# Kernel optimization log

Measured on AMD Instinct MI355X. Metric: run time of the kernel, lower is better.

The kernel has to match this reference:

```python
import jax, jax.numpy as jnp
import numpy as np

B, L, C, K, NLEV, VOCAB, OUT = 32, 1024, 512, 2, 4, 128, 11


def setup_inputs() -> dict:
    key = jax.random.key(0)
    ks = jax.random.split(key, 8)
    x = jax.random.randint(ks[0], (B, L), 0, VOCAB, dtype=jnp.int32)
    mask = jax.random.randint(ks[1], (B, L), 0, 2).astype(jnp.bool_)
    emb = jax.random.uniform(ks[2], (VOCAB, C), minval=-0.5, maxval=0.5, dtype=jnp.float32)
    w1 = jax.random.normal(ks[3], (NLEV, C, C, K), dtype=jnp.float32) * 0.02
    b1 = jnp.zeros((NLEV, C), dtype=jnp.float32)
    w2 = jax.random.normal(ks[4], (NLEV, C, C, K), dtype=jnp.float32) * 0.02
    b2 = jnp.zeros((NLEV, C), dtype=jnp.float32)
    dec_w = jax.random.uniform(ks[5], (OUT, C), minval=-0.5, maxval=0.5, dtype=jnp.float32)
    dec_b = jnp.zeros((OUT,), dtype=jnp.float32)
    return dict(x=x, mask=mask, emb=emb, w1=w1, b1=b1, w2=w2, b2=b2, dec_w=dec_w, dec_b=dec_b)


def _causal_conv(h, w, b, dilation):
    # h: [B, C, L], w: [Cout, Cin, K]; left-pad (K-1)*d == conv+chomp in TCN
    pad = (w.shape[-1] - 1) * dilation
    out = jax.lax.conv_general_dilated(
        h, w, window_strides=(1,), padding=[(pad, 0)],
        rhs_dilation=(dilation,), dimension_numbers=("NCH", "OIH", "NCH"))
    return out + b[None, :, None]


def reference(x, mask, emb, w1, b1, w2, b2, dec_w, dec_b):
    h = emb[x].transpose(0, 2, 1)  # [B, C, L]
    for i in range(NLEV):  # fixed small number of TCN levels
        d = 2 ** i
        res = h
        h = jax.nn.relu(_causal_conv(h, w1[i], b1[i], d))
        h = jax.nn.relu(_causal_conv(h, w2[i], b2[i], d))
        h = jax.nn.relu(h + res)  # residual (in==out channels -> identity shortcut)
    y = jnp.einsum("bcl,oc->blo", h, dec_w) + dec_b  # [B, L, OUT]
    # mask-gather: original keeps only mask-true positions; zero others (jit-safe)
    return y * mask[..., None].astype(y.dtype)
```

## Files before the change

kernel.cpp:

```cpp
#include <hip/hip_runtime.h>
#include <stdint.h>

#define BB 32
#define LL 1024
#define CC 512
#define NN (BB * LL)
#define NLEVS 4
#define OUTD 11
#define LPAD 8
#define LROWS (LL + LPAD)

typedef __attribute__((ext_vector_type(8))) short bf16x8;
typedef __attribute__((ext_vector_type(4))) float f32x4;

static __device__ __forceinline__ unsigned short f2bf(float f) {
    union { float f; uint32_t u; } v; v.f = f;
    uint32_t u = v.u;
    uint32_t r = (u + 0x7fffu + ((u >> 16) & 1u)) >> 16;
    return (unsigned short)r;
}
static __device__ __forceinline__ float bf2f(unsigned short h) {
    union { uint32_t u; float f; } v; v.u = ((uint32_t)h) << 16;
    return v.f;
}

static __device__ __forceinline__ void llds16(const unsigned short* g, unsigned short* l) {
    __builtin_amdgcn_global_load_lds(
        (const __attribute__((address_space(1))) unsigned int*)g,
        (__attribute__((address_space(3))) unsigned int*)l, 16, 0, 0);
}

__global__ __launch_bounds__(256) void prep_kernel(
    const int* __restrict__ x, const float* __restrict__ emb,
    const float* __restrict__ w1, const float* __restrict__ w2,
    const float* __restrict__ dw,
    unsigned short* __restrict__ Hb0, unsigned short* __restrict__ Hb1,
    unsigned short* __restrict__ WpT, unsigned short* __restrict__ dwp)
{
    int b = blockIdx.x;
    if (b < 16384) {
        int e = b * 256 + threadIdx.x;
        int cv = e >> 19;
        int r = e & 524287;
        int j = r >> 12;
        int co = (r >> 3) & 511;
        int h = r & 7;
        int kidx = j * 8 + h;
        int k = (kidx < 512) ? 1 : 0;
        int ci = kidx & 511;
        int lvl = cv >> 1;
        const float* w = (cv & 1) ? w2 : w1;
        WpT[e] = f2bf(w[(((size_t)(lvl * 512 + co) * 512) + ci) * 2 + k]);
    } else if (b < 24576) {
        int t = (b - 16384) * 256 + threadIdx.x;
        int n = t >> 6;
        int c8 = (t & 63) * 8;
        int idx = x[n];
        const float* src = emb + (size_t)idx * CC + c8;
        float4 v0 = *(const float4*)src;
        float4 v1 = *(const float4*)(src + 4);
        ushort4 a, bb;
        a.x = f2bf(v0.x); a.y = f2bf(v0.y); a.z = f2bf(v0.z); a.w = f2bf(v0.w);
        bb.x = f2bf(v1.x); bb.y = f2bf(v1.y); bb.z = f2bf(v1.z); bb.w = f2bf(v1.w);
        int prow = (n >> 10) * LROWS + LPAD + (n & (LL - 1));
        unsigned short* dst = Hb0 + (size_t)prow * CC + c8;
        *(ushort4*)dst = a;
        *(ushort4*)(dst + 4) = bb;
    } else if (b < 24704) {
        int t = (b - 24576) * 256 + threadIdx.x;
        unsigned short* base = (t >> 14) ? Hb1 : Hb0;
        int rem = t & 16383;
        int p = rem >> 9;
        int q = rem & 511;
        size_t off = (size_t)p * (LROWS * CC) + (size_t)q * 8;
        *(uint4*)(base + off) = (uint4){0u, 0u, 0u, 0u};
    } else {
        int e = (b - 24704) * 256 + threadIdx.x;
        int jb = e >> 7;
        int o = (e >> 3) & 15;
        int j = e & 7;
        dwp[e] = f2bf((o < OUTD) ? dw[o * CC + jb * 8 + j] : 0.f);
    }
}

#define PSEG 17
#define SROWS 136
#define PBUFH (SROWS * 64)
template <bool HAS_RES>
__global__ __launch_bounds__(256, 2) void conv_gemm(
    const unsigned short* __restrict__ Ain, const unsigned short* __restrict__ WpT,
    const float* __restrict__ bias, const unsigned short* __restrict__ resB,
    unsigned short* __restrict__ OutB, int d)
{
    __shared__ unsigned short sA[2 * 2 * PBUFH];
    __shared__ int s_flag[4][8];

    const int tid = threadIdx.x;
    const int wave = tid >> 6, lane = tid & 63;
    const int pairi = wave >> 1;

    const int bid = blockIdx.x;
    const int xcd = bid & 7;
    const int local = bid >> 3;
    const int cb = local >> 4;
    const int nb = xcd + 8 * (local & 15);
    const int co0 = cb * 128;
    const int n0 = nb * 256;

    const int rbase = (n0 >> 10) * LROWS + LPAD + (n0 & (LL - 1));
    const int wm = pairi * 128;
    const int wn = (wave & 1) * 64;
    const int lm = lane & 15, quad = lane >> 4;

    const int r8 = lane >> 3;
    const int c8 = lane & 7;

    if (tid < 32) ((int*)s_flag)[tid] = 0;
    __syncthreads();

    f32x4 acc[8][4];
#pragma unroll
    for (int i = 0; i < 8; ++i)
#pragma unroll
        for (int j = 0; j < 4; ++j) acc[i][j] = (f32x4){0.f, 0.f, 0.f, 0.f};

    unsigned short* pb = sA + pairi * (2 * PBUFH);
    const unsigned short* gAb =
        Ain + (size_t)(rbase - 8 + wm + r8) * CC + (c8 ^ r8) * 8;

    auto issue = [&](int it) {
        const unsigned short* gA = gAb + it * 64;
        unsigned short* lb = pb + (it & 1) * PBUFH;
#pragma unroll
        for (int seg = 0; seg < PSEG; ++seg)
            llds16(gA + (size_t)seg * 8 * CC, lb + seg * 512);
    };

    issue(0);

    bf16x8 breg[4][4];

    for (int it = 0; it < 8; ++it) {
        __builtin_amdgcn_s_waitcnt(0xF70);
        __asm__ volatile("" ::: "memory");

        const int jb0 = it * 8;
#pragma unroll
        for (int s = 0; s < 4; ++s) {
            const int t = s >> 1, ks = s & 1;
            const int jb = t * 64 + jb0 + ks * 4 + quad;
            const unsigned short* bbase = WpT + ((size_t)jb * 512 + co0 + wn + lm) * 8;
#pragma unroll
            for (int nt = 0; nt < 4; ++nt)
                breg[s][nt] = *(const bf16x8*)(bbase + (size_t)nt * 16 * 8);
        }
        __asm__ volatile("" ::: "memory");

        if (it < 7) {
            if (it >= 1) {
                volatile int* vp = &s_flag[wave ^ 1][it - 1];
                while (*vp == 0) __builtin_amdgcn_s_sleep(1);
            }
            issue(it + 1);
        }
        __asm__ volatile("" ::: "memory");

        const unsigned short* buf = pb + (it & 1) * PBUFH;

#pragma unroll
        for (int s = 0; s < 4; ++s) {
            const int t = s >> 1, ks = s & 1;
            const int shift = t ? d : 0;
            const int rowoff = 8 - shift;
            const int key = (8 - shift + lm) & 7;
            const int cpos = ((ks * 4 + quad) ^ key);
#pragma unroll
            for (int half = 0; half < 2; ++half) {
                bf16x8 af[4];
#pragma unroll
                for (int q = 0; q < 4; ++q) {
                    const int mt = half * 4 + q;
                    af[q] = *(const bf16x8*)&buf[(rowoff + mt * 16 + lm) * 64 + cpos * 8];
                }
#pragma unroll
                for (int q = 0; q < 4; ++q)
#pragma unroll
                    for (int nt = 0; nt < 4; ++nt)
                        acc[half * 4 + q][nt] = __builtin_amdgcn_mfma_f32_16x16x32_bf16(
                            af[q], breg[s][nt], acc[half * 4 + q][nt], 0, 0, 0);
            }
        }

        __asm__ volatile("" ::: "memory");
        if (lane == 0) *(volatile int*)&s_flag[wave][it] = 1;
    }

    float bv[4];
#pragma unroll
    for (int nt = 0; nt < 4; ++nt) bv[nt] = bias[co0 + wn + nt * 16 + lm];

#pragma unroll
    for (int mt = 0; mt < 8; ++mt) {
        int prow0 = rbase + wm + mt * 16 + quad * 4;
#pragma unroll
        for (int nt = 0; nt < 4; ++nt) {
            int co = co0 + wn + nt * 16 + lm;
#pragma unroll
            for (int r = 0; r < 4; ++r) {
                size_t off = (size_t)(prow0 + r) * CC + co;
                float v = acc[mt][nt][r] + bv[nt];
                v = fmaxf(v, 0.f);
                if (HAS_RES) {
                    v += bf2f(resB[off]);
                    v = fmaxf(v, 0.f);
                }
                OutB[off] = f2bf(v);
            }
        }
    }
}

__global__ __launch_bounds__(256) void decode_kernel(
    const unsigned short* __restrict__ H, const unsigned short* __restrict__ dwp,
    const float* __restrict__ db, const int* __restrict__ mask,
    float* __restrict__ out)
{
    const int wave = threadIdx.x >> 6, lane = threadIdx.x & 63;
    const int lm = lane & 15, quad = lane >> 4;
    const int n0 = blockIdx.x * 64 + wave * 16;
    const int prow = ((n0 + lm) >> 10) * LROWS + LPAD + ((n0 + lm) & (LL - 1));

    f32x4 acc = (f32x4){0.f, 0.f, 0.f, 0.f};
#pragma unroll
    for (int ks = 0; ks < 16; ++ks) {
        bf16x8 af = *(const bf16x8*)&H[(size_t)prow * CC + ks * 32 + quad * 8];
        bf16x8 bf = *(const bf16x8*)&dwp[((size_t)(ks * 4 + quad) * 16 + lm) * 8];
        acc = __builtin_amdgcn_mfma_f32_16x16x32_bf16(af, bf, acc, 0, 0, 0);
    }

    if (lm < OUTD) {
        float bo = db[lm];
#pragma unroll
        for (int r = 0; r < 4; ++r) {
            int n = n0 + quad * 4 + r;
            float v = (mask[n] != 0) ? (acc[r] + bo) : 0.f;
            out[(size_t)n * OUTD + lm] = v;
        }
    }
}

extern "C" void kernel_launch(void* const* d_in, const int* in_sizes, int n_in,
                              void* d_out, int out_size, void* d_ws, size_t ws_size,
                              hipStream_t stream)
{
    const int* x = (const int*)d_in[0];
    const int* mask = (const int*)d_in[1];
    const float* emb = (const float*)d_in[2];
    const float* w1 = (const float*)d_in[3];
    const float* b1 = (const float*)d_in[4];
    const float* w2 = (const float*)d_in[5];
    const float* b2 = (const float*)d_in[6];
    const float* dw = (const float*)d_in[7];
    const float* db = (const float*)d_in[8];
    float* out = (float*)d_out;

    char* ws = (char*)d_ws;
    const size_t HBB = (size_t)BB * LROWS * CC * 2;
    unsigned short* Hb0 = (unsigned short*)ws;
    unsigned short* Hb1 = (unsigned short*)(ws + HBB);
    unsigned short* WpT = (unsigned short*)(ws + 2 * HBB);
    unsigned short* dwp = (unsigned short*)(ws + 2 * HBB + (size_t)NLEVS * 2 * CC * 1024 * 2);

    prep_kernel<<<24736, 256, 0, stream>>>(x, emb, w1, w2, dw, Hb0, Hb1, WpT, dwp);

    const int grid = (CC / 128) * (NN / 256);
    for (int i = 0; i < NLEVS; ++i) {
        int d = 1 << i;
        const unsigned short* W1 = WpT + (size_t)(i * 2 + 0) * CC * 1024;
        const unsigned short* W2 = WpT + (size_t)(i * 2 + 1) * CC * 1024;
        conv_gemm<false><<<grid, 256, 0, stream>>>(Hb0, W1, b1 + i * CC, nullptr, Hb1, d);
        conv_gemm<true><<<grid, 256, 0, stream>>>(Hb1, W2, b2 + i * CC, Hb0, Hb0, d);
    }
    decode_kernel<<<NN / 64, 256, 0, stream>>>(Hb0, dwp, db, mask, out);
}
```

Baseline: 393.5 us.

## Widen conv GEMM blocks to 512 threads with 256 output channels and barrier ping-pong

Each conv GEMM block grows to 8 waves covering 256 output channels, so each staged A tile in LDS is reused across twice as many output columns and the grid halves. The per-pair spin-flag sync is replaced by s_barrier, and the global-to-LDS loads of each tile are split across the four waves of a group. The MFMA loop is reorganised into barrier-separated phases with s_setprio to interleave LDS reads and MFMA work across waves. The risks are added barrier stalls, higher register pressure under 512-thread launch bounds, and the hand-written waitcnt encodings needing to be exactly right.

```diff
diff --git a/kernel.cpp b/kernel.cpp
--- a/kernel.cpp
+++ b/kernel.cpp
@@ -83,57 +83,55 @@
     }
 }
 
-#define PSEG 17
 #define SROWS 136
 #define PBUFH (SROWS * 64)
 template <bool HAS_RES>
-__global__ __launch_bounds__(256, 2) void conv_gemm(
+__global__ __launch_bounds__(512, 2) void conv_gemm(
     const unsigned short* __restrict__ Ain, const unsigned short* __restrict__ WpT,
     const float* __restrict__ bias, const unsigned short* __restrict__ resB,
     unsigned short* __restrict__ OutB, int d)
 {
     __shared__ unsigned short sA[2 * 2 * PBUFH];
-    __shared__ int s_flag[4][8];
 
     const int tid = threadIdx.x;
     const int wave = tid >> 6, lane = tid & 63;
-    const int pairi = wave >> 1;
+    const int g = wave >> 2;
+    const int ws = wave & 3;
 
     const int bid = blockIdx.x;
     const int xcd = bid & 7;
     const int local = bid >> 3;
     const int cb = local >> 4;
     const int nb = xcd + 8 * (local & 15);
-    const int co0 = cb * 128;
+    const int co0 = cb * 256;
     const int n0 = nb * 256;
 
     const int rbase = (n0 >> 10) * LROWS + LPAD + (n0 & (LL - 1));
-    const int wm = pairi * 128;
-    const int wn = (wave & 1) * 64;
+    const int wm = g * 128;
+    const int wn = ws * 64;
     const int lm = lane & 15, quad = lane >> 4;
 
     const int r8 = lane >> 3;
     const int c8 = lane & 7;
 
-    if (tid < 32) ((int*)s_flag)[tid] = 0;
-    __syncthreads();
-
     f32x4 acc[8][4];
 #pragma unroll
     for (int i = 0; i < 8; ++i)
 #pragma unroll
         for (int j = 0; j < 4; ++j) acc[i][j] = (f32x4){0.f, 0.f, 0.f, 0.f};
 
-    unsigned short* pb = sA + pairi * (2 * PBUFH);
+    unsigned short* pb = sA + g * (2 * PBUFH);
     const unsigned short* gAb =
         Ain + (size_t)(rbase - 8 + wm + r8) * CC + (c8 ^ r8) * 8;
 
     auto issue = [&](int it) {
         const unsigned short* gA = gAb + it * 64;
         unsigned short* lb = pb + (it & 1) * PBUFH;
-#pragma unroll
-        for (int seg = 0; seg < PSEG; ++seg)
-            llds16(gA + (size_t)seg * 8 * CC, lb + seg * 512);
+        llds16(gA + (size_t)(ws + 0) * 8 * CC, lb + (ws + 0) * 512);
+        llds16(gA + (size_t)(ws + 4) * 8 * CC, lb + (ws + 4) * 512);
+        llds16(gA + (size_t)(ws + 8) * 8 * CC, lb + (ws + 8) * 512);
+        llds16(gA + (size_t)(ws + 12) * 8 * CC, lb + (ws + 12) * 512);
+        if (ws == 0) llds16(gA + (size_t)16 * 8 * CC, lb + 16 * 512);
     };
 
     issue(0);
@@ -141,9 +139,6 @@
     bf16x8 breg[4][4];
 
     for (int it = 0; it < 8; ++it) {
-        __builtin_amdgcn_s_waitcnt(0xF70);
-        __asm__ volatile("" ::: "memory");
-
         const int jb0 = it * 8;
 #pragma unroll
         for (int s = 0; s < 4; ++s) {
@@ -154,45 +149,47 @@
             for (int nt = 0; nt < 4; ++nt)
                 breg[s][nt] = *(const bf16x8*)(bbase + (size_t)nt * 16 * 8);
         }
+
+        if (it < 7) {
+            issue(it + 1);
+            if (ws == 0) __builtin_amdgcn_s_waitcnt(0x4F75);
+            else         __builtin_amdgcn_s_waitcnt(0x4F74);
+        } else {
+            __builtin_amdgcn_s_waitcnt(0x4F70);
+        }
         __asm__ volatile("" ::: "memory");
-
-        if (it < 7) {
-            if (it >= 1) {
-                volatile int* vp = &s_flag[wave ^ 1][it - 1];
-                while (*vp == 0) __builtin_amdgcn_s_sleep(1);
-            }
-            issue(it + 1);
-        }
+        __builtin_amdgcn_s_barrier();
         __asm__ volatile("" ::: "memory");
 
         const unsigned short* buf = pb + (it & 1) * PBUFH;
 
 #pragma unroll
-        for (int s = 0; s < 4; ++s) {
+        for (int p = 0; p < 8; ++p) {
+            const int s = p >> 1, hsel = p & 1;
             const int t = s >> 1, ks = s & 1;
             const int shift = t ? d : 0;
             const int rowoff = 8 - shift;
             const int key = (8 - shift + lm) & 7;
             const int cpos = ((ks * 4 + quad) ^ key);
-#pragma unroll
-            for (int half = 0; half < 2; ++half) {
-                bf16x8 af[4];
-#pragma unroll
-                for (int q = 0; q < 4; ++q) {
-                    const int mt = half * 4 + q;
-                    af[q] = *(const bf16x8*)&buf[(rowoff + mt * 16 + lm) * 64 + cpos * 8];
-                }
-#pragma unroll
-                for (int q = 0; q < 4; ++q)
-#pragma unroll
-                    for (int nt = 0; nt < 4; ++nt)
-                        acc[half * 4 + q][nt] = __builtin_amdgcn_mfma_f32_16x16x32_bf16(
-                            af[q], breg[s][nt], acc[half * 4 + q][nt], 0, 0, 0);
+            bf16x8 af[4];
+#pragma unroll
+            for (int q = 0; q < 4; ++q) {
+                const int mt = hsel * 4 + q;
+                af[q] = *(const bf16x8*)&buf[(rowoff + mt * 16 + lm) * 64 + cpos * 8];
             }
-        }
-
-        __asm__ volatile("" ::: "memory");
-        if (lane == 0) *(volatile int*)&s_flag[wave][it] = 1;
+            __builtin_amdgcn_s_barrier();
+            __builtin_amdgcn_s_waitcnt(0xC07F);
+            __builtin_amdgcn_sched_barrier(0);
+            __builtin_amdgcn_s_setprio(1);
+#pragma unroll
+            for (int q = 0; q < 4; ++q)
+#pragma unroll
+                for (int nt = 0; nt < 4; ++nt)
+                    acc[hsel * 4 + q][nt] = __builtin_amdgcn_mfma_f32_16x16x32_bf16(
+                        af[q], breg[s][nt], acc[hsel * 4 + q][nt], 0, 0, 0);
+            __builtin_amdgcn_s_setprio(0);
+            __builtin_amdgcn_s_barrier();
+        }
     }
 
     float bv[4];
@@ -273,13 +270,13 @@
 
     prep_kernel<<<24736, 256, 0, stream>>>(x, emb, w1, w2, dw, Hb0, Hb1, WpT, dwp);
 
-    const int grid = (CC / 128) * (NN / 256);
+    const int grid = (CC / 256) * (NN / 256);
     for (int i = 0; i < NLEVS; ++i) {
         int d = 1 << i;
         const unsigned short* W1 = WpT + (size_t)(i * 2 + 0) * CC * 1024;
         const unsigned short* W2 = WpT + (size_t)(i * 2 + 1) * CC * 1024;
-        conv_gemm<false><<<grid, 256, 0, stream>>>(Hb0, W1, b1 + i * CC, nullptr, Hb1, d);
-        conv_gemm<true><<<grid, 256, 0, stream>>>(Hb1, W2, b2 + i * CC, Hb0, Hb0, d);
+        conv_gemm<false><<<grid, 512, 0, stream>>>(Hb0, W1, b1 + i * CC, nullptr, Hb1, d);
+        conv_gemm<true><<<grid, 512, 0, stream>>>(Hb1, W2, b2 + i * CC, Hb0, Hb0, d);
     }
     decode_kernel<<<NN / 64, 256, 0, stream>>>(Hb0, dwp, db, mask, out);
 }
```

After: 424.3 us. 7.8% more time.
